# Optimization experiments

Measured on AMD Instinct MI355X. Metric: run time of the kernel, lower is better.

## Reference

```python
import jax, jax.numpy as jnp
import numpy as np
from jax import lax

B, DIM, H, W = 4, 256, 128, 128
KS, LOC, STRIDES_CFG, HEADS = 5, [2, 3], [1, 2], 8
C2 = DIM // 2
GK = HEADS * KS  # per-pixel dynamic kernel channels

def _kernel_map(ks, kstride, kloc):
    # replicates LSAMixer.generate_kernel_map_1d
    axes, strides, start = [0], [1], 1
    for loc, s in zip(kloc, kstride):
        for num in range(0, loc - start):
            axes.append(num * s + axes[-1] + strides[-1])
            strides.append(s)
        start = loc
    patch = (axes[-1] + strides[-1]) * 2 - 1
    full_axes = [-a for a in axes[:0:-1]] + axes
    full_strides = strides[:0:-1] + strides
    return full_axes, full_strides, patch

OFFS, STRDS, PATCH = _kernel_map(KS, STRIDES_CFG, LOC)
PAD = PATCH // 2

def _pw(x, w, b):
    # 1x1 conv as GEMM
    return jnp.einsum('bchw,oc->bohw', x, w) + b[None, :, None, None]

def _dw(x, w, b, ph, pw):
    # depthwise conv, torch OIHW layout with I=1
    y = lax.conv_general_dilated(x, w, (1, 1), [(ph, ph), (pw, pw)],
                                 feature_group_count=x.shape[1],
                                 dimension_numbers=('NCHW', 'OIHW', 'NCHW'))
    return y + b[None, :, None, None]

def _fsa(x, kern, groups, axis):
    # dynamic local attention: for each tap k (offset a, stride s) gather the
    # average of x over the s-wide strided window along `axis`, weight it by
    # the per-head dynamic kernel, and accumulate.
    Bx, Cx, Hx, Wx = x.shape
    gd = Cx // groups
    K = len(OFFS)
    L = x.shape[axis]
    padcfg = [(0, 0)] * 4
    padcfg[axis] = (PAD, PAD)
    xp = jnp.pad(x, padcfg)
    taps = []
    for a, s in zip(OFFS, STRDS):
        start = a if a >= 0 else a - s + 1  # window covers s pixels away from center
        acc = lax.slice_in_dim(xp, PAD + start, PAD + start + L, axis=axis)
        for d in range(1, s):
            acc = acc + lax.slice_in_dim(xp, PAD + start + d, PAD + start + d + L, axis=axis)
        taps.append(acc / s)
    t = jnp.stack(taps, 0).reshape(K, Bx, groups, gd, Hx, Wx)
    k = kern.reshape(Bx, groups, K, Hx, Wx)
    return jnp.einsum('kbgdhw,bgkhw->bgdhw', t, k).reshape(Bx, Cx, Hx, Wx)

def setup_inputs() -> dict:
    key = jax.random.key(0)
    ks = jax.random.split(key, 12)
    sc = 0.02
    f32 = jnp.float32
    return {
        'x': jax.random.normal(ks[0], (B, DIM, H, W), f32),
        'proj_in_w': jax.random.normal(ks[1], (DIM, DIM), f32) * sc,
        'proj_in_b': jnp.zeros((DIM,), f32),
        'hk_dw_w': jax.random.normal(ks[2], (C2, 1, 1, PATCH), f32) * sc,
        'hk_dw_b': jnp.zeros((C2,), f32),
        'hk_pw_w': jax.random.normal(ks[3], (GK, C2), f32) * sc,
        'hk_pw_b': jnp.zeros((GK,), f32),
        'vk_dw_w': jax.random.normal(ks[4], (C2, 1, PATCH, 1), f32) * sc,
        'vk_dw_b': jnp.zeros((C2,), f32),
        'vk_pw_w': jax.random.normal(ks[5], (GK, C2), f32) * sc,
        'vk_pw_b': jnp.zeros((GK,), f32),
        'cb_w1': jax.random.normal(ks[6], (DIM // 4, C2), f32) * sc,
        'cb_b1': jnp.zeros((DIM // 4,), f32),
        'cb_w2': jax.random.normal(ks[7], (C2, DIM // 4), f32) * sc,
        'cb_b2': jnp.zeros((C2,), f32),
        'proj_out_w': jax.random.normal(ks[8], (DIM, DIM), f32) * sc,
        'proj_out_b': jnp.zeros((DIM,), f32),
    }

def reference(x, proj_in_w, proj_in_b, hk_dw_w, hk_dw_b, hk_pw_w, hk_pw_b,
              vk_dw_w, vk_dw_b, vk_pw_w, vk_pw_b, cb_w1, cb_b1, cb_w2, cb_b2,
              proj_out_w, proj_out_b):
    Bv, _, Hv, Wv = x.shape
    h = _pw(x, proj_in_w, proj_in_b)
    x1, x2 = h[:, :C2], h[:, C2:]
    # channel branch: pw -> relu -> pw
    x_conv = _pw(jax.nn.relu(_pw(x1, cb_w1, cb_b1)), cb_w2, cb_b2)
    # horizontal dynamic kernel + fsa
    kh = jnp.tanh(_pw(_dw(x2, hk_dw_w, hk_dw_b, 0, PAD), hk_pw_w, hk_pw_b))
    attn_h = _fsa(x2, kh, HEADS, axis=3)
    # vertical dynamic kernel + fsa
    kv = jnp.tanh(_pw(_dw(attn_h, vk_dw_w, vk_dw_b, PAD, 0), vk_pw_w, vk_pw_b))
    attn = _fsa(attn_h, kv, HEADS, axis=2)
    N = Hv * Wv
    xc = x_conv.reshape(Bv, C2, N)
    at = attn.reshape(Bv, C2, N)
    # SpatialInteraction(x_conv, attn): modulates x_conv
    s_sig = jax.nn.sigmoid(jnp.einsum('bc,bcn->bn', at.mean(-1), xc) / C2)[:, None, :]
    spatial_map = (s_sig * xc).reshape(Bv, C2, Hv, Wv)
    # ChannelInteraction(x_conv, attn): modulates attn
    c_sig = jax.nn.sigmoid(jnp.einsum('bcn,bn->bc', at, xc.mean(1)) / N)[:, :, None]
    channel_map = (c_sig * at).reshape(Bv, C2, Hv, Wv)
    out = jnp.concatenate([spatial_map, channel_map], axis=1)
    return _pw(out, proj_out_w, proj_out_b)
```

## Files before the change

kernel.cpp:

```cpp
#include <hip/hip_runtime.h>
#include <hip/hip_bf16.h>
#include <math.h>

typedef __hip_bfloat16 bf16;
typedef __attribute__((ext_vector_type(8))) short short8;
typedef __attribute__((ext_vector_type(4))) float floatx4;
#define DEV __device__ __forceinline__

constexpr int BATCH = 4;
constexpr int DIM   = 256;
constexpr int C2    = 128;
constexpr int GK    = 40;
constexpr int HH    = 128;
constexpr int WW    = 128;
constexpr int NPIX  = HH * WW;
constexpr int TPB   = 256;

DEV float toF(float v) { return v; }
DEV float toF(bf16 v)  { return __bfloat162float(v); }

DEV unsigned short f2bs(float f) {
  union { bf16 h; unsigned short u; } cv;
  cv.h = __float2bfloat16(f);
  return cv.u;
}
DEV float bs2f(unsigned short u) {
  union { float f; unsigned x; } c;
  c.x = ((unsigned)u) << 16;
  return c.f;
}

template<int N>
DEV void load_f32v(const float* __restrict__ p, float* v) {
  if constexpr (N == 8) {
    const float4 a = *(const float4*)p;
    const float4 b = *(const float4*)(p + 4);
    v[0]=a.x; v[1]=a.y; v[2]=a.z; v[3]=a.w; v[4]=b.x; v[5]=b.y; v[6]=b.z; v[7]=b.w;
  } else if constexpr (N == 4) {
    const float4 a = *(const float4*)p;
    v[0]=a.x; v[1]=a.y; v[2]=a.z; v[3]=a.w;
  } else {
    const float2 a = *(const float2*)p;
    v[0]=a.x; v[1]=a.y;
  }
}
template<int N>
DEV void load_bf16v(const bf16* __restrict__ p, float* v) {
  if constexpr (N == 8) {
    const uint4 u = *(const uint4*)p;
    v[0]=bs2f(u.x & 0xffff); v[1]=bs2f(u.x >> 16);
    v[2]=bs2f(u.y & 0xffff); v[3]=bs2f(u.y >> 16);
    v[4]=bs2f(u.z & 0xffff); v[5]=bs2f(u.z >> 16);
    v[6]=bs2f(u.w & 0xffff); v[7]=bs2f(u.w >> 16);
  } else if constexpr (N == 4) {
    const uint2 u = *(const uint2*)p;
    v[0]=bs2f(u.x & 0xffff); v[1]=bs2f(u.x >> 16);
    v[2]=bs2f(u.y & 0xffff); v[3]=bs2f(u.y >> 16);
  } else {
    const unsigned u = *(const unsigned*)p;
    v[0]=bs2f(u & 0xffff); v[1]=bs2f(u >> 16);
  }
}
DEV void load8bf(const bf16* __restrict__ p, float* v) { load_bf16v<8>(p, v); }

__global__ __launch_bounds__(TPB) void prepack_kernel(
    const float* __restrict__ w0, const float* __restrict__ w1,
    const float* __restrict__ w2, const float* __restrict__ w3,
    const float* __restrict__ w4, const float* __restrict__ w5,
    short* __restrict__ dst) {
  const int i = blockIdx.x * TPB + threadIdx.x;
  if (i >= 157696) return;
  int j = i;
  float v;
  if (j < 65536) v = w0[j];
  else if ((j -= 65536) < 8192) v = w1[j];
  else if ((j -= 8192) < 8192) v = w2[j];
  else if ((j -= 8192) < 5120) v = w3[j];
  else if ((j -= 5120) < 5120) v = w4[j];
  else { j -= 5120; v = w5[j]; }
  dst[i] = (short)f2bs(v);
}

template<int K, int O, int ACT, int GATED, typename TIN, typename TOUT>
__global__ __launch_bounds__(TPB) void pw2_kernel(
    const TIN* __restrict__ in, int in_bs,
    const short* __restrict__ wbf, const float* __restrict__ bias,
    TOUT* __restrict__ out, int out_bs,
    const bf16* __restrict__ gxc, const bf16* __restrict__ gattn,
    const float* __restrict__ gs, const float* __restrict__ gc) {
  constexpr int C8   = K / 8;
  constexpr int PXT  = K / 32;
  constexpr int PG   = 64 / PXT;
  constexpr int ROWB = K * 2 + 16;
  constexpr int WO   = (O + 63) / 64;
  __shared__ char smem[64 * ROWB];

  const int p0   = blockIdx.x * 64;
  const int b    = blockIdx.y;
  const int t    = threadIdx.x;
  const int lane = t & 63, wid = t >> 6;
  const int q    = lane >> 4, i16 = lane & 15;

  {
    const int c8  = t / PG;
    const int px0 = (t % PG) * PXT;
    float vals[8][PXT];
    float svals[PXT];
    if constexpr (GATED) {
      if (c8 < C8 / 2) load_f32v<PXT>(gs + (size_t)b * NPIX + p0 + px0, svals);
    }
#pragma unroll
    for (int j = 0; j < 8; ++j) {
      const int c = c8 * 8 + j;
      float tmp[PXT];
      if constexpr (GATED) {
        if (c < C2) {
          load_bf16v<PXT>(gxc + ((size_t)b * C2 + c) * NPIX + p0 + px0, tmp);
#pragma unroll
          for (int px = 0; px < PXT; ++px) vals[j][px] = tmp[px] * svals[px];
        } else {
          const float cg = gc[b * C2 + (c - C2)];
          load_bf16v<PXT>(gattn + ((size_t)b * C2 + (c - C2)) * NPIX + p0 + px0, tmp);
#pragma unroll
          for (int px = 0; px < PXT; ++px) vals[j][px] = tmp[px] * cg;
        }
      } else {
        const TIN* src = in + ((size_t)b * in_bs + c) * NPIX + p0 + px0;
        if constexpr (sizeof(TIN) == 4) load_f32v<PXT>((const float*)src, tmp);
        else                            load_bf16v<PXT>((const bf16*)src, tmp);
#pragma unroll
        for (int px = 0; px < PXT; ++px) vals[j][px] = tmp[px];
      }
    }
#pragma unroll
    for (int px = 0; px < PXT; ++px) {
      const int p = px0 + px;
      short8 pk;
#pragma unroll
      for (int j = 0; j < 8; ++j) pk[j] = (short)f2bs(vals[j][px]);
      const int phys = c8 ^ ((p >> 3) & 7);
      *reinterpret_cast<short8*>(smem + (size_t)p * ROWB + phys * 16) = pk;
    }
  }
  __syncthreads();

  const int o_base = wid * WO * 16;
  if (o_base >= O) return;

  floatx4 acc[WO][4];
#pragma unroll
  for (int ot = 0; ot < WO; ++ot)
#pragma unroll
    for (int nt = 0; nt < 4; ++nt)
      acc[ot][nt] = (floatx4){0.f, 0.f, 0.f, 0.f};

  for (int kc = 0; kc < K / 32; ++kc) {
    short8 afrag[WO];
#pragma unroll
    for (int ot = 0; ot < WO; ++ot) {
      int o = o_base + ot * 16 + i16;
      if (o >= O) o = O - 1;
      afrag[ot] = *reinterpret_cast<const short8*>(wbf + (size_t)o * K + kc * 32 + q * 8);
    }
    short8 bfrag[4];
#pragma unroll
    for (int nt = 0; nt < 4; ++nt) {
      const int n = nt * 16 + i16;
      const int phys = (kc * 4 + q) ^ ((n >> 3) & 7);
      bfrag[nt] = *reinterpret_cast<const short8*>(smem + (size_t)n * ROWB + phys * 16);
    }
#pragma unroll
    for (int ot = 0; ot < WO; ++ot)
#pragma unroll
      for (int nt = 0; nt < 4; ++nt)
        acc[ot][nt] = __builtin_amdgcn_mfma_f32_16x16x32_bf16(
            afrag[ot], bfrag[nt], acc[ot][nt], 0, 0, 0);
  }

#pragma unroll
  for (int ot = 0; ot < WO; ++ot) {
#pragma unroll
    for (int reg = 0; reg < 4; ++reg) {
      const int o = o_base + ot * 16 + q * 4 + reg;
      if (o < O) {
        const float bv = bias[o];
#pragma unroll
        for (int nt = 0; nt < 4; ++nt) {
          float v = acc[ot][nt][reg] + bv;
          if (ACT == 1) v = fmaxf(v, 0.0f);
          if (ACT == 2) v = tanhf(v);
          TOUT* dst = out + ((size_t)b * out_bs + o) * NPIX + p0 + nt * 16 + i16;
          if constexpr (sizeof(TOUT) == 4) *dst = v;
          else *dst = __float2bfloat16(v);
        }
      }
    }
  }
}

__global__ __launch_bounds__(TPB) void dwh2_kernel(
    const float* __restrict__ in, int in_bs,
    const float* __restrict__ w7, const float* __restrict__ bias,
    bf16* __restrict__ out) {
  const int g  = blockIdx.x * TPB + threadIdx.x;
  const int w8 = g & 15;
  const int hp = (g >> 4) & (HH - 1);
  const int c  = (g >> 11) & (C2 - 1);
  const int b  = g >> 18;
  const float* xr = in + ((size_t)b * in_bs + c) * NPIX + hp * WW;
  const int px0 = w8 * 8;
  float xs[14];
  if (w8 > 0) { const float4 L = *(const float4*)(xr + px0 - 4); xs[0]=L.y; xs[1]=L.z; xs[2]=L.w; }
  else { xs[0]=xs[1]=xs[2]=0.f; }
  { const float4 a = *(const float4*)(xr + px0);
    const float4 bq = *(const float4*)(xr + px0 + 4);
    xs[3]=a.x; xs[4]=a.y; xs[5]=a.z; xs[6]=a.w;
    xs[7]=bq.x; xs[8]=bq.y; xs[9]=bq.z; xs[10]=bq.w; }
  if (w8 < 15) { const float4 R = *(const float4*)(xr + px0 + 8); xs[11]=R.x; xs[12]=R.y; xs[13]=R.z; }
  else { xs[11]=xs[12]=xs[13]=0.f; }
  float wv[7];
#pragma unroll
  for (int j = 0; j < 7; ++j) wv[j] = w7[c * 7 + j];
  const float bv = bias[c];
  short8 o;
#pragma unroll
  for (int i = 0; i < 8; ++i) {
    float a = bv;
#pragma unroll
    for (int j = 0; j < 7; ++j) a = fmaf(wv[j], xs[i + j], a);
    o[i] = (short)f2bs(a);
  }
  *reinterpret_cast<short8*>(out + ((size_t)(b * C2 + c)) * NPIX + hp * WW + px0) = o;
}

__global__ __launch_bounds__(TPB) void dwv2_kernel(
    const bf16* __restrict__ in,
    const float* __restrict__ w7, const float* __restrict__ bias,
    bf16* __restrict__ out) {
  const int g  = blockIdx.x * TPB + threadIdx.x;
  const int w8 = g & 15;
  const int hp = (g >> 4) & (HH - 1);
  const int c  = (g >> 11) & (C2 - 1);
  const int b  = g >> 18;
  const int px0 = w8 * 8;
  const bf16* base = in + ((size_t)(b * C2 + c)) * NPIX + px0;
  float r[7][8];
#pragma unroll
  for (int j = 0; j < 7; ++j) {
    const int hq = hp - 3 + j;
    if (hq >= 0 && hq < HH) load8bf(base + (size_t)hq * WW, r[j]);
    else
#pragma unroll
      for (int i = 0; i < 8; ++i) r[j][i] = 0.f;
  }
  float wv[7];
#pragma unroll
  for (int j = 0; j < 7; ++j) wv[j] = w7[c * 7 + j];
  const float bv = bias[c];
  short8 o;
#pragma unroll
  for (int i = 0; i < 8; ++i) {
    float a = bv;
#pragma unroll
    for (int j = 0; j < 7; ++j) a = fmaf(wv[j], r[j][i], a);
    o[i] = (short)f2bs(a);
  }
  *reinterpret_cast<short8*>(out + ((size_t)(b * C2 + c)) * NPIX + hp * WW + px0) = o;
}

__global__ __launch_bounds__(TPB) void fsah2_kernel(
    const float* __restrict__ x, int x_bs,
    const bf16* __restrict__ kern, bf16* __restrict__ out) {
  const int g  = blockIdx.x * TPB + threadIdx.x;
  const int w8 = g & 15;
  const int hp = (g >> 4) & (HH - 1);
  const int c  = (g >> 11) & (C2 - 1);
  const int b  = g >> 18;
  const float* xr = x + ((size_t)b * x_bs + c) * NPIX + hp * WW;
  const int px0 = w8 * 8;
  float xs[14];
  if (w8 > 0) { const float4 L = *(const float4*)(xr + px0 - 4); xs[0]=L.y; xs[1]=L.z; xs[2]=L.w; }
  else { xs[0]=xs[1]=xs[2]=0.f; }
  { const float4 a = *(const float4*)(xr + px0);
    const float4 bq = *(const float4*)(xr + px0 + 4);
    xs[3]=a.x; xs[4]=a.y; xs[5]=a.z; xs[6]=a.w;
    xs[7]=bq.x; xs[8]=bq.y; xs[9]=bq.z; xs[10]=bq.w; }
  if (w8 < 15) { const float4 R = *(const float4*)(xr + px0 + 8); xs[11]=R.x; xs[12]=R.y; xs[13]=R.z; }
  else { xs[11]=xs[12]=xs[13]=0.f; }
  float k[5][8];
  const bf16* kr = kern + ((size_t)b * GK + (c >> 4) * 5) * NPIX + hp * WW + px0;
#pragma unroll
  for (int tp = 0; tp < 5; ++tp) load8bf(kr + (size_t)tp * NPIX, k[tp]);
  short8 o;
#pragma unroll
  for (int i = 0; i < 8; ++i) {
    float a = 0.5f * (xs[i] + xs[i + 1]) * k[0][i];
    a = fmaf(xs[i + 2], k[1][i], a);
    a = fmaf(xs[i + 3], k[2][i], a);
    a = fmaf(xs[i + 4], k[3][i], a);
    a = fmaf(0.5f * (xs[i + 5] + xs[i + 6]), k[4][i], a);
    o[i] = (short)f2bs(a);
  }
  *reinterpret_cast<short8*>(out + ((size_t)(b * C2 + c)) * NPIX + hp * WW + px0) = o;
}

__global__ __launch_bounds__(TPB) void fsav2_kernel(
    const bf16* __restrict__ x,
    const bf16* __restrict__ kern, bf16* __restrict__ out) {
  const int g  = blockIdx.x * TPB + threadIdx.x;
  const int w8 = g & 15;
  const int hp = (g >> 4) & (HH - 1);
  const int c  = (g >> 11) & (C2 - 1);
  const int b  = g >> 18;
  const int px0 = w8 * 8;
  const bf16* base = x + ((size_t)(b * C2 + c)) * NPIX + px0;
  float r[7][8];
#pragma unroll
  for (int j = 0; j < 7; ++j) {
    const int hq = hp - 3 + j;
    if (hq >= 0 && hq < HH) load8bf(base + (size_t)hq * WW, r[j]);
    else
#pragma unroll
      for (int i = 0; i < 8; ++i) r[j][i] = 0.f;
  }
  float k[5][8];
  const bf16* kr = kern + ((size_t)b * GK + (c >> 4) * 5) * NPIX + hp * WW + px0;
#pragma unroll
  for (int tp = 0; tp < 5; ++tp) load8bf(kr + (size_t)tp * NPIX, k[tp]);
  short8 o;
#pragma unroll
  for (int i = 0; i < 8; ++i) {
    float a = 0.5f * (r[0][i] + r[1][i]) * k[0][i];
    a = fmaf(r[2][i], k[1][i], a);
    a = fmaf(r[3][i], k[2][i], a);
    a = fmaf(r[4][i], k[3][i], a);
    a = fmaf(0.5f * (r[5][i] + r[6][i]), k[4][i], a);
    o[i] = (short)f2bs(a);
  }
  *reinterpret_cast<short8*>(out + ((size_t)(b * C2 + c)) * NPIX + hp * WW + px0) = o;
}

DEV float block_reduce_sum(float v) {
#pragma unroll
  for (int off = 32; off > 0; off >>= 1) v += __shfl_down(v, off, 64);
  __shared__ float ls[TPB / 64];
  const int lane = threadIdx.x & 63;
  const int wid  = threadIdx.x >> 6;
  if (lane == 0) ls[wid] = v;
  __syncthreads();
  float s = 0.0f;
  if (threadIdx.x == 0) {
#pragma unroll
    for (int i = 0; i < TPB / 64; ++i) s += ls[i];
  }
  return s;
}

__global__ __launch_bounds__(TPB) void mean_n_kernel(const bf16* __restrict__ in,
                                                     float* __restrict__ out) {
  const int bc = blockIdx.x;
  const bf16* r = in + (size_t)bc * NPIX;
  float s = 0.0f;
  for (int i = threadIdx.x * 8; i < NPIX; i += TPB * 8) {
    float v[8];
    load8bf(r + i, v);
#pragma unroll
    for (int j = 0; j < 8; ++j) s += v[j];
  }
  s = block_reduce_sum(s);
  if (threadIdx.x == 0) out[bc] = s * (1.0f / NPIX);
}

__global__ __launch_bounds__(TPB) void xcmean_kernel(const bf16* __restrict__ xc,
                                                     float* __restrict__ out) {
  const int p = blockIdx.x * TPB + threadIdx.x;
  const int b = blockIdx.y;
  const bf16* r = xc + (size_t)b * C2 * NPIX + p;
  float s = 0.0f;
#pragma unroll 4
  for (int c = 0; c < C2; ++c) s += toF(r[(size_t)c * NPIX]);
  out[(size_t)b * NPIX + p] = s * (1.0f / C2);
}

__global__ __launch_bounds__(TPB) void ssig_kernel(const bf16* __restrict__ xc,
                                                   const float* __restrict__ at_mean,
                                                   float* __restrict__ out) {
  __shared__ float am[C2];
  const int b = blockIdx.y;
  if (threadIdx.x < C2) am[threadIdx.x] = at_mean[b * C2 + threadIdx.x];
  __syncthreads();
  const int p = blockIdx.x * TPB + threadIdx.x;
  const bf16* r = xc + (size_t)b * C2 * NPIX + p;
  float s = 0.0f;
#pragma unroll 4
  for (int c = 0; c < C2; ++c) s = fmaf(am[c], toF(r[(size_t)c * NPIX]), s);
  out[(size_t)b * NPIX + p] = 1.0f / (1.0f + expf(-s * (1.0f / C2)));
}

__global__ __launch_bounds__(TPB) void csig_kernel(const bf16* __restrict__ attn,
                                                   const float* __restrict__ xc_mean,
                                                   float* __restrict__ out) {
  const int bc = blockIdx.x;
  const int b  = bc / C2;
  const bf16* r = attn + (size_t)bc * NPIX;
  const float* m = xc_mean + (size_t)b * NPIX;
  float s = 0.0f;
  for (int i = threadIdx.x * 8; i < NPIX; i += TPB * 8) {
    float v[8], mm[8];
    load8bf(r + i, v);
    load_f32v<8>(m + i, mm);
#pragma unroll
    for (int j = 0; j < 8; ++j) s = fmaf(v[j], mm[j], s);
  }
  s = block_reduce_sum(s);
  if (threadIdx.x == 0) out[bc] = 1.0f / (1.0f + expf(-s * (1.0f / NPIX)));
}

extern "C" void kernel_launch(void* const* d_in, const int* in_sizes, int n_in,
                              void* d_out, int out_size, void* d_ws, size_t ws_size,
                              hipStream_t stream) {
  const float* x    = (const float*)d_in[0];
  const float* piw  = (const float*)d_in[1];
  const float* pib  = (const float*)d_in[2];
  const float* hkdw = (const float*)d_in[3];
  const float* hkdb = (const float*)d_in[4];
  const float* hkpw = (const float*)d_in[5];
  const float* hkpb = (const float*)d_in[6];
  const float* vkdw = (const float*)d_in[7];
  const float* vkdb = (const float*)d_in[8];
  const float* vkpw = (const float*)d_in[9];
  const float* vkpb = (const float*)d_in[10];
  const float* cbw1 = (const float*)d_in[11];
  const float* cbb1 = (const float*)d_in[12];
  const float* cbw2 = (const float*)d_in[13];
  const float* cbb2 = (const float*)d_in[14];
  const float* pow_ = (const float*)d_in[15];
  const float* pob  = (const float*)d_in[16];
  float* out = (float*)d_out;

  char* ws = (char*)d_ws;
  size_t off = 0;
  auto alloc = [&](size_t bytes) -> char* {
    char* p = ws + off;
    off += (bytes + 255) & ~(size_t)255;
    return p;
  };
  short* wpk    = (short*)alloc(157696 * 2);
  float* h      = (float*)alloc((size_t)BATCH * DIM * NPIX * 4);
  bf16*  t1     = (bf16*) alloc((size_t)BATCH * 64  * NPIX * 2);
  bf16*  x_conv = (bf16*) alloc((size_t)BATCH * C2  * NPIX * 2);
  bf16*  dwbuf  = (bf16*) alloc((size_t)BATCH * C2  * NPIX * 2);
  bf16*  kbuf   = (bf16*) alloc((size_t)BATCH * GK  * NPIX * 2);
  bf16*  attn_h = (bf16*) alloc((size_t)BATCH * C2  * NPIX * 2);
  bf16*  attn   = (bf16*) alloc((size_t)BATCH * C2  * NPIX * 2);
  float* at_mean = (float*)alloc((size_t)BATCH * C2 * 4);
  float* xc_mean = (float*)alloc((size_t)BATCH * NPIX * 4);
  float* s_sig   = (float*)alloc((size_t)BATCH * NPIX * 4);
  float* c_sig   = (float*)alloc((size_t)BATCH * C2 * 4);

  const short* w_pi  = wpk;
  const short* w_cb1 = wpk + 65536;
  const short* w_cb2 = wpk + 73728;
  const short* w_hk  = wpk + 81920;
  const short* w_vk  = wpk + 87040;
  const short* w_po  = wpk + 92160;

  const dim3 blk(TPB);
  const dim3 gemm_grid(NPIX / 64, BATCH);
  const int PT  = NPIX / TPB;
  const int EL8 = BATCH * C2 * HH * 16 / TPB;
  const float* x2 = h + (size_t)C2 * NPIX;

  prepack_kernel<<<dim3((157696 + TPB - 1) / TPB), blk, 0, stream>>>(
      piw, cbw1, cbw2, hkpw, vkpw, pow_, wpk);
  pw2_kernel<256, 256, 0, 0, float, float><<<gemm_grid, blk, 0, stream>>>(
      x, DIM, w_pi, pib, h, DIM, nullptr, nullptr, nullptr, nullptr);
  pw2_kernel<128, 64, 1, 0, float, bf16><<<gemm_grid, blk, 0, stream>>>(
      h, DIM, w_cb1, cbb1, t1, 64, nullptr, nullptr, nullptr, nullptr);
  pw2_kernel<64, 128, 0, 0, bf16, bf16><<<gemm_grid, blk, 0, stream>>>(
      t1, 64, w_cb2, cbb2, x_conv, C2, nullptr, nullptr, nullptr, nullptr);
  dwh2_kernel<<<dim3(EL8), blk, 0, stream>>>(x2, DIM, hkdw, hkdb, dwbuf);
  pw2_kernel<128, 40, 2, 0, bf16, bf16><<<gemm_grid, blk, 0, stream>>>(
      dwbuf, C2, w_hk, hkpb, kbuf, GK, nullptr, nullptr, nullptr, nullptr);
  fsah2_kernel<<<dim3(EL8), blk, 0, stream>>>(x2, DIM, kbuf, attn_h);
  dwv2_kernel<<<dim3(EL8), blk, 0, stream>>>(attn_h, vkdw, vkdb, dwbuf);
  pw2_kernel<128, 40, 2, 0, bf16, bf16><<<gemm_grid, blk, 0, stream>>>(
      dwbuf, C2, w_vk, vkpb, kbuf, GK, nullptr, nullptr, nullptr, nullptr);
  fsav2_kernel<<<dim3(EL8), blk, 0, stream>>>(attn_h, kbuf, attn);
  mean_n_kernel<<<dim3(BATCH * C2), blk, 0, stream>>>(attn, at_mean);
  xcmean_kernel<<<dim3(PT, BATCH), blk, 0, stream>>>(x_conv, xc_mean);
  ssig_kernel<<<dim3(PT, BATCH), blk, 0, stream>>>(x_conv, at_mean, s_sig);
  csig_kernel<<<dim3(BATCH * C2), blk, 0, stream>>>(attn, xc_mean, c_sig);
  pw2_kernel<256, 256, 0, 1, bf16, float><<<gemm_grid, blk, 0, stream>>>(
      x_conv, 0, w_po, pob, out, DIM, x_conv, attn, s_sig, c_sig);
}
```

Measured before the change: 304.9 us.

## Split output channels across blocks in big GEMMs, chunk staging, fuse xc reductions

The two 256x256 pointwise GEMMs now split their output channels across two blocks per pixel tile, which doubles the grid. Each block re-stages the same input tile into shared memory. The staging loop is processed in chunks of up to 4 pixels to cut register pressure, and launch bounds now request 4 blocks per CU to raise occupancy. The xc mean and spatial sigmoid kernels are fused into one pass over x_conv, which removes a full read of that tensor. The cost is duplicated input loads and conversion work in the split GEMMs.

Result: slower. 316.1 us (+3.7%).

```diff
diff --git a/kernel.cpp b/kernel.cpp
--- a/kernel.cpp
+++ b/kernel.cpp
@@ -81,8 +81,8 @@
   dst[i] = (short)f2bs(v);
 }
 
-template<int K, int O, int ACT, int GATED, typename TIN, typename TOUT>
-__global__ __launch_bounds__(TPB) void pw2_kernel(
+template<int K, int O, int OSPL, int ACT, int GATED, typename TIN, typename TOUT>
+__global__ __launch_bounds__(TPB, 4) void pw2_kernel(
     const TIN* __restrict__ in, int in_bs,
     const short* __restrict__ wbf, const float* __restrict__ bias,
     TOUT* __restrict__ out, int out_bs,
@@ -92,10 +92,14 @@
   constexpr int PXT  = K / 32;
   constexpr int PG   = 64 / PXT;
   constexpr int ROWB = K * 2 + 16;
-  constexpr int WO   = (O + 63) / 64;
+  constexpr int OB   = O / OSPL;
+  constexpr int WO   = (OB + 63) / 64;
+  constexpr int CH   = (PXT < 4) ? PXT : 4;
   __shared__ char smem[64 * ROWB];
 
-  const int p0   = blockIdx.x * 64;
+  const int bx   = blockIdx.x;
+  const int oz   = (OSPL > 1) ? (bx % OSPL) : 0;
+  const int p0   = ((OSPL > 1) ? (bx / OSPL) : bx) * 64;
   const int b    = blockIdx.y;
   const int t    = threadIdx.x;
   const int lane = t & 63, wid = t >> 6;
@@ -104,48 +108,51 @@
   {
     const int c8  = t / PG;
     const int px0 = (t % PG) * PXT;
-    float vals[8][PXT];
-    float svals[PXT];
-    if constexpr (GATED) {
-      if (c8 < C8 / 2) load_f32v<PXT>(gs + (size_t)b * NPIX + p0 + px0, svals);
-    }
-#pragma unroll
-    for (int j = 0; j < 8; ++j) {
-      const int c = c8 * 8 + j;
-      float tmp[PXT];
+#pragma unroll
+    for (int pc = 0; pc < PXT; pc += CH) {
+      float vals[8][CH];
+      float svals[CH];
       if constexpr (GATED) {
-        if (c < C2) {
-          load_bf16v<PXT>(gxc + ((size_t)b * C2 + c) * NPIX + p0 + px0, tmp);
-#pragma unroll
-          for (int px = 0; px < PXT; ++px) vals[j][px] = tmp[px] * svals[px];
+        if (c8 < C8 / 2) load_f32v<CH>(gs + (size_t)b * NPIX + p0 + px0 + pc, svals);
+      }
+#pragma unroll
+      for (int j = 0; j < 8; ++j) {
+        const int c = c8 * 8 + j;
+        float tmp[CH];
+        if constexpr (GATED) {
+          if (c < C2) {
+            load_bf16v<CH>(gxc + ((size_t)b * C2 + c) * NPIX + p0 + px0 + pc, tmp);
+#pragma unroll
+            for (int px = 0; px < CH; ++px) vals[j][px] = tmp[px] * svals[px];
+          } else {
+            const float cg = gc[b * C2 + (c - C2)];
+            load_bf16v<CH>(gattn + ((size_t)b * C2 + (c - C2)) * NPIX + p0 + px0 + pc, tmp);
+#pragma unroll
+            for (int px = 0; px < CH; ++px) vals[j][px] = tmp[px] * cg;
+          }
         } else {
-          const float cg = gc[b * C2 + (c - C2)];
-          load_bf16v<PXT>(gattn + ((size_t)b * C2 + (c - C2)) * NPIX + p0 + px0, tmp);
-#pragma unroll
-          for (int px = 0; px < PXT; ++px) vals[j][px] = tmp[px] * cg;
+          const TIN* src = in + ((size_t)b * in_bs + c) * NPIX + p0 + px0 + pc;
+          if constexpr (sizeof(TIN) == 4) load_f32v<CH>((const float*)src, tmp);
+          else                            load_bf16v<CH>((const bf16*)src, tmp);
+#pragma unroll
+          for (int px = 0; px < CH; ++px) vals[j][px] = tmp[px];
         }
-      } else {
-        const TIN* src = in + ((size_t)b * in_bs + c) * NPIX + p0 + px0;
-        if constexpr (sizeof(TIN) == 4) load_f32v<PXT>((const float*)src, tmp);
-        else                            load_bf16v<PXT>((const bf16*)src, tmp);
-#pragma unroll
-        for (int px = 0; px < PXT; ++px) vals[j][px] = tmp[px];
+      }
+#pragma unroll
+      for (int px = 0; px < CH; ++px) {
+        const int p = px0 + pc + px;
+        short8 pk;
+#pragma unroll
+        for (int j = 0; j < 8; ++j) pk[j] = (short)f2bs(vals[j][px]);
+        const int phys = c8 ^ ((p >> 3) & 7);
+        *reinterpret_cast<short8*>(smem + (size_t)p * ROWB + phys * 16) = pk;
       }
     }
-#pragma unroll
-    for (int px = 0; px < PXT; ++px) {
-      const int p = px0 + px;
-      short8 pk;
-#pragma unroll
-      for (int j = 0; j < 8; ++j) pk[j] = (short)f2bs(vals[j][px]);
-      const int phys = c8 ^ ((p >> 3) & 7);
-      *reinterpret_cast<short8*>(smem + (size_t)p * ROWB + phys * 16) = pk;
-    }
   }
   __syncthreads();
 
-  const int o_base = wid * WO * 16;
-  if (o_base >= O) return;
+  if (wid * WO * 16 >= OB) return;
+  const int o_base = oz * OB + wid * WO * 16;
 
   floatx4 acc[WO][4];
 #pragma unroll
@@ -371,30 +378,25 @@
   if (threadIdx.x == 0) out[bc] = s * (1.0f / NPIX);
 }
 
-__global__ __launch_bounds__(TPB) void xcmean_kernel(const bf16* __restrict__ xc,
-                                                     float* __restrict__ out) {
-  const int p = blockIdx.x * TPB + threadIdx.x;
-  const int b = blockIdx.y;
-  const bf16* r = xc + (size_t)b * C2 * NPIX + p;
-  float s = 0.0f;
-#pragma unroll 4
-  for (int c = 0; c < C2; ++c) s += toF(r[(size_t)c * NPIX]);
-  out[(size_t)b * NPIX + p] = s * (1.0f / C2);
-}
-
-__global__ __launch_bounds__(TPB) void ssig_kernel(const bf16* __restrict__ xc,
-                                                   const float* __restrict__ at_mean,
-                                                   float* __restrict__ out) {
+__global__ __launch_bounds__(TPB) void xs_kernel(const bf16* __restrict__ xc,
+                                                 const float* __restrict__ at_mean,
+                                                 float* __restrict__ xc_mean,
+                                                 float* __restrict__ s_sig) {
   __shared__ float am[C2];
   const int b = blockIdx.y;
   if (threadIdx.x < C2) am[threadIdx.x] = at_mean[b * C2 + threadIdx.x];
   __syncthreads();
   const int p = blockIdx.x * TPB + threadIdx.x;
   const bf16* r = xc + (size_t)b * C2 * NPIX + p;
-  float s = 0.0f;
+  float s = 0.0f, m = 0.0f;
 #pragma unroll 4
-  for (int c = 0; c < C2; ++c) s = fmaf(am[c], toF(r[(size_t)c * NPIX]), s);
-  out[(size_t)b * NPIX + p] = 1.0f / (1.0f + expf(-s * (1.0f / C2)));
+  for (int c = 0; c < C2; ++c) {
+    const float v = toF(r[(size_t)c * NPIX]);
+    m += v;
+    s = fmaf(am[c], v, s);
+  }
+  xc_mean[(size_t)b * NPIX + p] = m * (1.0f / C2);
+  s_sig[(size_t)b * NPIX + p]   = 1.0f / (1.0f + expf(-s * (1.0f / C2)));
 }
 
 __global__ __launch_bounds__(TPB) void csig_kernel(const bf16* __restrict__ attn,
@@ -467,30 +469,30 @@
 
   const dim3 blk(TPB);
   const dim3 gemm_grid(NPIX / 64, BATCH);
+  const dim3 gemm_grid2(NPIX / 64 * 2, BATCH);
   const int PT  = NPIX / TPB;
   const int EL8 = BATCH * C2 * HH * 16 / TPB;
   const float* x2 = h + (size_t)C2 * NPIX;
 
   prepack_kernel<<<dim3((157696 + TPB - 1) / TPB), blk, 0, stream>>>(
       piw, cbw1, cbw2, hkpw, vkpw, pow_, wpk);
-  pw2_kernel<256, 256, 0, 0, float, float><<<gemm_grid, blk, 0, stream>>>(
+  pw2_kernel<256, 256, 2, 0, 0, float, float><<<gemm_grid2, blk, 0, stream>>>(
       x, DIM, w_pi, pib, h, DIM, nullptr, nullptr, nullptr, nullptr);
-  pw2_kernel<128, 64, 1, 0, float, bf16><<<gemm_grid, blk, 0, stream>>>(
+  pw2_kernel<128, 64, 1, 1, 0, float, bf16><<<gemm_grid, blk, 0, stream>>>(
       h, DIM, w_cb1, cbb1, t1, 64, nullptr, nullptr, nullptr, nullptr);
-  pw2_kernel<64, 128, 0, 0, bf16, bf16><<<gemm_grid, blk, 0, stream>>>(
+  pw2_kernel<64, 128, 1, 0, 0, bf16, bf16><<<gemm_grid, blk, 0, stream>>>(
       t1, 64, w_cb2, cbb2, x_conv, C2, nullptr, nullptr, nullptr, nullptr);
   dwh2_kernel<<<dim3(EL8), blk, 0, stream>>>(x2, DIM, hkdw, hkdb, dwbuf);
-  pw2_kernel<128, 40, 2, 0, bf16, bf16><<<gemm_grid, blk, 0, stream>>>(
+  pw2_kernel<128, 40, 1, 2, 0, bf16, bf16><<<gemm_grid, blk, 0, stream>>>(
       dwbuf, C2, w_hk, hkpb, kbuf, GK, nullptr, nullptr, nullptr, nullptr);
   fsah2_kernel<<<dim3(EL8), blk, 0, stream>>>(x2, DIM, kbuf, attn_h);
   dwv2_kernel<<<dim3(EL8), blk, 0, stream>>>(attn_h, vkdw, vkdb, dwbuf);
-  pw2_kernel<128, 40, 2, 0, bf16, bf16><<<gemm_grid, blk, 0, stream>>>(
+  pw2_kernel<128, 40, 1, 2, 0, bf16, bf16><<<gemm_grid, blk, 0, stream>>>(
       dwbuf, C2, w_vk, vkpb, kbuf, GK, nullptr, nullptr, nullptr, nullptr);
   fsav2_kernel<<<dim3(EL8), blk, 0, stream>>>(attn_h, kbuf, attn);
   mean_n_kernel<<<dim3(BATCH * C2), blk, 0, stream>>>(attn, at_mean);
-  xcmean_kernel<<<dim3(PT, BATCH), blk, 0, stream>>>(x_conv, xc_mean);
-  ssig_kernel<<<dim3(PT, BATCH), blk, 0, stream>>>(x_conv, at_mean, s_sig);
+  xs_kernel<<<dim3(PT, BATCH), blk, 0, stream>>>(x_conv, at_mean, xc_mean, s_sig);
   csig_kernel<<<dim3(BATCH * C2), blk, 0, stream>>>(attn, xc_mean, c_sig);
-  pw2_kernel<256, 256, 0, 1, bf16, float><<<gemm_grid, blk, 0, stream>>>(
+  pw2_kernel<256, 256, 2, 0, 1, bf16, float><<<gemm_grid2, blk, 0, stream>>>(
       x_conv, 0, w_po, pob, out, DIM, x_conv, attn, s_sig, c_sig);
 }
```

## Double-buffer pointwise GEMM tiles and fuse xc-mean with spatial sigmoid

Applied to the files above, without the earlier changes.

Each pointwise-conv GEMM block now processes two 64-pixel tiles and ping-pongs between two shared-memory buffers. The global loads for the next tile are issued before the MFMA compute on the current tile, so load latency can overlap with math. The launch grid is halved to match. Separately, the xc_mean and s_sig reductions over x_conv are merged into one kernel, so x_conv is read once and one launch is dropped. The trade-offs are more register pressure from keeping prefetched values live, with launch_bounds now asking for 2 blocks per CU, doubled LDS per block, and fewer blocks in flight.

New measurement: 314.8 us. +3.3%, slower.

```diff
diff --git a/kernel.cpp b/kernel.cpp
--- a/kernel.cpp
+++ b/kernel.cpp
@@ -81,8 +81,8 @@
   dst[i] = (short)f2bs(v);
 }
 
-template<int K, int O, int ACT, int GATED, typename TIN, typename TOUT>
-__global__ __launch_bounds__(TPB) void pw2_kernel(
+template<int K, int O, int T, int ACT, int GATED, typename TIN, typename TOUT>
+__global__ __launch_bounds__(TPB, 2) void pw3_kernel(
     const TIN* __restrict__ in, int in_bs,
     const short* __restrict__ wbf, const float* __restrict__ bias,
     TOUT* __restrict__ out, int out_bs,
@@ -92,19 +92,21 @@
   constexpr int PXT  = K / 32;
   constexpr int PG   = 64 / PXT;
   constexpr int ROWB = K * 2 + 16;
+  constexpr int BUFB = 64 * ROWB;
   constexpr int WO   = (O + 63) / 64;
-  __shared__ char smem[64 * ROWB];
-
-  const int p0   = blockIdx.x * 64;
+  __shared__ char smem[2 * BUFB];
+
   const int b    = blockIdx.y;
   const int t    = threadIdx.x;
   const int lane = t & 63, wid = t >> 6;
   const int q    = lane >> 4, i16 = lane & 15;
-
-  {
-    const int c8  = t / PG;
-    const int px0 = (t % PG) * PXT;
-    float vals[8][PXT];
+  const int c8   = t / PG;
+  const int px0  = (t % PG) * PXT;
+  const int o_base = wid * WO * 16;
+
+  float vals[8][PXT];
+
+  auto stage_load = [&](int p0) {
     float svals[PXT];
     if constexpr (GATED) {
       if (c8 < C8 / 2) load_f32v<PXT>(gs + (size_t)b * NPIX + p0 + px0, svals);
@@ -112,8 +114,8 @@
 #pragma unroll
     for (int j = 0; j < 8; ++j) {
       const int c = c8 * 8 + j;
-      float tmp[PXT];
       if constexpr (GATED) {
+        float tmp[PXT];
         if (c < C2) {
           load_bf16v<PXT>(gxc + ((size_t)b * C2 + c) * NPIX + p0 + px0, tmp);
 #pragma unroll
@@ -126,12 +128,13 @@
         }
       } else {
         const TIN* src = in + ((size_t)b * in_bs + c) * NPIX + p0 + px0;
-        if constexpr (sizeof(TIN) == 4) load_f32v<PXT>((const float*)src, tmp);
-        else                            load_bf16v<PXT>((const bf16*)src, tmp);
-#pragma unroll
-        for (int px = 0; px < PXT; ++px) vals[j][px] = tmp[px];
+        if constexpr (sizeof(TIN) == 4) load_f32v<PXT>((const float*)src, vals[j]);
+        else                            load_bf16v<PXT>((const bf16*)src, vals[j]);
       }
     }
+  };
+
+  auto stage_write = [&](char* buf) {
 #pragma unroll
     for (int px = 0; px < PXT; ++px) {
       const int p = px0 + px;
@@ -139,62 +142,73 @@
 #pragma unroll
       for (int j = 0; j < 8; ++j) pk[j] = (short)f2bs(vals[j][px]);
       const int phys = c8 ^ ((p >> 3) & 7);
-      *reinterpret_cast<short8*>(smem + (size_t)p * ROWB + phys * 16) = pk;
+      *reinterpret_cast<short8*>(buf + (size_t)p * ROWB + phys * 16) = pk;
     }
-  }
-  __syncthreads();
-
-  const int o_base = wid * WO * 16;
-  if (o_base >= O) return;
-
-  floatx4 acc[WO][4];
-#pragma unroll
-  for (int ot = 0; ot < WO; ++ot)
-#pragma unroll
-    for (int nt = 0; nt < 4; ++nt)
-      acc[ot][nt] = (floatx4){0.f, 0.f, 0.f, 0.f};
-
-  for (int kc = 0; kc < K / 32; ++kc) {
-    short8 afrag[WO];
+  };
+
+  auto compute_store = [&](const char* buf, int p0) {
+    floatx4 acc[WO][4];
+#pragma unroll
+    for (int ot = 0; ot < WO; ++ot)
+#pragma unroll
+      for (int nt = 0; nt < 4; ++nt)
+        acc[ot][nt] = (floatx4){0.f, 0.f, 0.f, 0.f};
+
+    for (int kc = 0; kc < K / 32; ++kc) {
+      short8 afrag[WO];
+#pragma unroll
+      for (int ot = 0; ot < WO; ++ot) {
+        int o = o_base + ot * 16 + i16;
+        if (o >= O) o = O - 1;
+        afrag[ot] = *reinterpret_cast<const short8*>(wbf + (size_t)o * K + kc * 32 + q * 8);
+      }
+      short8 bfrag[4];
+#pragma unroll
+      for (int nt = 0; nt < 4; ++nt) {
+        const int n = nt * 16 + i16;
+        const int phys = (kc * 4 + q) ^ ((n >> 3) & 7);
+        bfrag[nt] = *reinterpret_cast<const short8*>(buf + (size_t)n * ROWB + phys * 16);
+      }
+#pragma unroll
+      for (int ot = 0; ot < WO; ++ot)
+#pragma unroll
+        for (int nt = 0; nt < 4; ++nt)
+          acc[ot][nt] = __builtin_amdgcn_mfma_f32_16x16x32_bf16(
+              afrag[ot], bfrag[nt], acc[ot][nt], 0, 0, 0);
+    }
+
 #pragma unroll
     for (int ot = 0; ot < WO; ++ot) {
-      int o = o_base + ot * 16 + i16;
-      if (o >= O) o = O - 1;
-      afrag[ot] = *reinterpret_cast<const short8*>(wbf + (size_t)o * K + kc * 32 + q * 8);
-    }
-    short8 bfrag[4];
-#pragma unroll
-    for (int nt = 0; nt < 4; ++nt) {
-      const int n = nt * 16 + i16;
-      const int phys = (kc * 4 + q) ^ ((n >> 3) & 7);
-      bfrag[nt] = *reinterpret_cast<const short8*>(smem + (size_t)n * ROWB + phys * 16);
-    }
-#pragma unroll
-    for (int ot = 0; ot < WO; ++ot)
-#pragma unroll
-      for (int nt = 0; nt < 4; ++nt)
-        acc[ot][nt] = __builtin_amdgcn_mfma_f32_16x16x32_bf16(
-            afrag[ot], bfrag[nt], acc[ot][nt], 0, 0, 0);
-  }
-
-#pragma unroll
-  for (int ot = 0; ot < WO; ++ot) {
-#pragma unroll
-    for (int reg = 0; reg < 4; ++reg) {
-      const int o = o_base + ot * 16 + q * 4 + reg;
-      if (o < O) {
-        const float bv = bias[o];
-#pragma unroll
-        for (int nt = 0; nt < 4; ++nt) {
-          float v = acc[ot][nt][reg] + bv;
-          if (ACT == 1) v = fmaxf(v, 0.0f);
-          if (ACT == 2) v = tanhf(v);
-          TOUT* dst = out + ((size_t)b * out_bs + o) * NPIX + p0 + nt * 16 + i16;
-          if constexpr (sizeof(TOUT) == 4) *dst = v;
-          else *dst = __float2bfloat16(v);
+#pragma unroll
+      for (int reg = 0; reg < 4; ++reg) {
+        const int o = o_base + ot * 16 + q * 4 + reg;
+        if (o < O) {
+          const float bv = bias[o];
+#pragma unroll
+          for (int nt = 0; nt < 4; ++nt) {
+            float v = acc[ot][nt][reg] + bv;
+            if (ACT == 1) v = fmaxf(v, 0.0f);
+            if (ACT == 2) v = tanhf(v);
+            TOUT* dst = out + ((size_t)b * out_bs + o) * NPIX + p0 + nt * 16 + i16;
+            if constexpr (sizeof(TOUT) == 4) *dst = v;
+            else *dst = __float2bfloat16(v);
+          }
         }
       }
     }
+  };
+
+  const int p_base = blockIdx.x * T * 64;
+
+  stage_load(p_base);
+  stage_write(smem);
+  __syncthreads();
+
+  for (int tt = 0; tt < T; ++tt) {
+    if (tt + 1 < T) stage_load(p_base + (tt + 1) * 64);
+    if (o_base < O) compute_store(smem + (tt & 1) * BUFB, p_base + tt * 64);
+    if (tt + 1 < T) stage_write(smem + ((tt + 1) & 1) * BUFB);
+    __syncthreads();
   }
 }
 
@@ -371,30 +385,25 @@
   if (threadIdx.x == 0) out[bc] = s * (1.0f / NPIX);
 }
 
-__global__ __launch_bounds__(TPB) void xcmean_kernel(const bf16* __restrict__ xc,
-                                                     float* __restrict__ out) {
-  const int p = blockIdx.x * TPB + threadIdx.x;
-  const int b = blockIdx.y;
-  const bf16* r = xc + (size_t)b * C2 * NPIX + p;
-  float s = 0.0f;
-#pragma unroll 4
-  for (int c = 0; c < C2; ++c) s += toF(r[(size_t)c * NPIX]);
-  out[(size_t)b * NPIX + p] = s * (1.0f / C2);
-}
-
-__global__ __launch_bounds__(TPB) void ssig_kernel(const bf16* __restrict__ xc,
-                                                   const float* __restrict__ at_mean,
-                                                   float* __restrict__ out) {
+__global__ __launch_bounds__(TPB) void xs_kernel(const bf16* __restrict__ xc,
+                                                 const float* __restrict__ at_mean,
+                                                 float* __restrict__ xc_mean,
+                                                 float* __restrict__ s_sig) {
   __shared__ float am[C2];
   const int b = blockIdx.y;
   if (threadIdx.x < C2) am[threadIdx.x] = at_mean[b * C2 + threadIdx.x];
   __syncthreads();
   const int p = blockIdx.x * TPB + threadIdx.x;
   const bf16* r = xc + (size_t)b * C2 * NPIX + p;
-  float s = 0.0f;
+  float s = 0.0f, m = 0.0f;
 #pragma unroll 4
-  for (int c = 0; c < C2; ++c) s = fmaf(am[c], toF(r[(size_t)c * NPIX]), s);
-  out[(size_t)b * NPIX + p] = 1.0f / (1.0f + expf(-s * (1.0f / C2)));
+  for (int c = 0; c < C2; ++c) {
+    const float v = toF(r[(size_t)c * NPIX]);
+    m += v;
+    s = fmaf(am[c], v, s);
+  }
+  xc_mean[(size_t)b * NPIX + p] = m * (1.0f / C2);
+  s_sig[(size_t)b * NPIX + p]   = 1.0f / (1.0f + expf(-s * (1.0f / C2)));
 }
 
 __global__ __launch_bounds__(TPB) void csig_kernel(const bf16* __restrict__ attn,
@@ -466,31 +475,31 @@
   const short* w_po  = wpk + 92160;
 
   const dim3 blk(TPB);
-  const dim3 gemm_grid(NPIX / 64, BATCH);
+  constexpr int TLS = 2;
+  const dim3 gemm_grid(NPIX / 64 / TLS, BATCH);
   const int PT  = NPIX / TPB;
   const int EL8 = BATCH * C2 * HH * 16 / TPB;
   const float* x2 = h + (size_t)C2 * NPIX;
 
   prepack_kernel<<<dim3((157696 + TPB - 1) / TPB), blk, 0, stream>>>(
       piw, cbw1, cbw2, hkpw, vkpw, pow_, wpk);
-  pw2_kernel<256, 256, 0, 0, float, float><<<gemm_grid, blk, 0, stream>>>(
+  pw3_kernel<256, 256, TLS, 0, 0, float, float><<<gemm_grid, blk, 0, stream>>>(
       x, DIM, w_pi, pib, h, DIM, nullptr, nullptr, nullptr, nullptr);
-  pw2_kernel<128, 64, 1, 0, float, bf16><<<gemm_grid, blk, 0, stream>>>(
+  pw3_kernel<128, 64, TLS, 1, 0, float, bf16><<<gemm_grid, blk, 0, stream>>>(
       h, DIM, w_cb1, cbb1, t1, 64, nullptr, nullptr, nullptr, nullptr);
-  pw2_kernel<64, 128, 0, 0, bf16, bf16><<<gemm_grid, blk, 0, stream>>>(
+  pw3_kernel<64, 128, TLS, 0, 0, bf16, bf16><<<gemm_grid, blk, 0, stream>>>(
       t1, 64, w_cb2, cbb2, x_conv, C2, nullptr, nullptr, nullptr, nullptr);
   dwh2_kernel<<<dim3(EL8), blk, 0, stream>>>(x2, DIM, hkdw, hkdb, dwbuf);
-  pw2_kernel<128, 40, 2, 0, bf16, bf16><<<gemm_grid, blk, 0, stream>>>(
+  pw3_kernel<128, 40, TLS, 2, 0, bf16, bf16><<<gemm_grid, blk, 0, stream>>>(
       dwbuf, C2, w_hk, hkpb, kbuf, GK, nullptr, nullptr, nullptr, nullptr);
   fsah2_kernel<<<dim3(EL8), blk, 0, stream>>>(x2, DIM, kbuf, attn_h);
   dwv2_kernel<<<dim3(EL8), blk, 0, stream>>>(attn_h, vkdw, vkdb, dwbuf);
-  pw2_kernel<128, 40, 2, 0, bf16, bf16><<<gemm_grid, blk, 0, stream>>>(
+  pw3_kernel<128, 40, TLS, 2, 0, bf16, bf16><<<gemm_grid, blk, 0, stream>>>(
       dwbuf, C2, w_vk, vkpb, kbuf, GK, nullptr, nullptr, nullptr, nullptr);
   fsav2_kernel<<<dim3(EL8), blk, 0, stream>>>(attn_h, kbuf, attn);
   mean_n_kernel<<<dim3(BATCH * C2), blk, 0, stream>>>(attn, at_mean);
-  xcmean_kernel<<<dim3(PT, BATCH), blk, 0, stream>>>(x_conv, xc_mean);
-  ssig_kernel<<<dim3(PT, BATCH), blk, 0, stream>>>(x_conv, at_mean, s_sig);
+  xs_kernel<<<dim3(PT, BATCH), blk, 0, stream>>>(x_conv, at_mean, xc_mean, s_sig);
   csig_kernel<<<dim3(BATCH * C2), blk, 0, stream>>>(attn, xc_mean, c_sig);
-  pw2_kernel<256, 256, 0, 1, bf16, float><<<gemm_grid, blk, 0, stream>>>(
+  pw3_kernel<256, 256, TLS, 0, 1, bf16, float><<<gemm_grid, blk, 0, stream>>>(
       x_conv, 0, w_po, pob, out, DIM, x_conv, attn, s_sig, c_sig);
 }
```

## Fuse proj_in and channel-branch GEMMs into one kernel; merge xc mean and spatial sigmoid

Applied to the files above, without the earlier changes.

Adds a single kernel that runs the input projection, the first channel-branch pointwise conv with ReLU, and the second pointwise conv back to back. The x1 half and the intermediate t1 stay in shared memory as bf16, so the full fp32 h tensor and t1 are never written to or re-read from global memory. Only x2 is written out in fp32 for the later depthwise and attention stages. It also merges the xc mean and s_sig reductions into one pass over x_conv. The cost is a larger shared-memory footprint per block, which may lower occupancy.

Measured after the change: 283.9 us. 1.07x faster.

```diff
diff --git a/kernel.cpp b/kernel.cpp
--- a/kernel.cpp
+++ b/kernel.cpp
@@ -193,6 +193,191 @@
           if constexpr (sizeof(TOUT) == 4) *dst = v;
           else *dst = __float2bfloat16(v);
         }
+      }
+    }
+  }
+}
+
+__global__ __launch_bounds__(TPB) void pwfused_kernel(
+    const float* __restrict__ x,
+    const short* __restrict__ w_pi, const float* __restrict__ pib,
+    const short* __restrict__ w_cb1, const float* __restrict__ cbb1,
+    const short* __restrict__ w_cb2, const float* __restrict__ cbb2,
+    float* __restrict__ x2out, bf16* __restrict__ xconv) {
+  constexpr int ROWB  = 256 * 2 + 16;
+  constexpr int HROWB = 128 * 2 + 16;
+  constexpr int TROWB = 64 * 2 + 16;
+  __shared__ char smem[64 * ROWB];
+  __shared__ char hbuf[64 * HROWB];
+  __shared__ char tbuf[64 * TROWB];
+
+  const int p0   = blockIdx.x * 64;
+  const int b    = blockIdx.y;
+  const int t    = threadIdx.x;
+  const int lane = t & 63, wid = t >> 6;
+  const int q    = lane >> 4, i16 = lane & 15;
+
+  {
+    const int c8  = t / 8;
+    const int px0 = (t % 8) * 8;
+    float vals[8][8];
+#pragma unroll
+    for (int j = 0; j < 8; ++j) {
+      const int c = c8 * 8 + j;
+      load_f32v<8>(x + ((size_t)b * DIM + c) * NPIX + p0 + px0, vals[j]);
+    }
+#pragma unroll
+    for (int px = 0; px < 8; ++px) {
+      const int p = px0 + px;
+      short8 pk;
+#pragma unroll
+      for (int j = 0; j < 8; ++j) pk[j] = (short)f2bs(vals[j][px]);
+      const int phys = c8 ^ ((p >> 3) & 7);
+      *reinterpret_cast<short8*>(smem + (size_t)p * ROWB + phys * 16) = pk;
+    }
+  }
+  __syncthreads();
+
+  const int o_base = wid * 64;
+  {
+    floatx4 acc[4][4];
+#pragma unroll
+    for (int ot = 0; ot < 4; ++ot)
+#pragma unroll
+      for (int nt = 0; nt < 4; ++nt)
+        acc[ot][nt] = (floatx4){0.f, 0.f, 0.f, 0.f};
+
+    for (int kc = 0; kc < 8; ++kc) {
+      short8 afrag[4];
+#pragma unroll
+      for (int ot = 0; ot < 4; ++ot) {
+        const int o = o_base + ot * 16 + i16;
+        afrag[ot] = *reinterpret_cast<const short8*>(w_pi + (size_t)o * 256 + kc * 32 + q * 8);
+      }
+      short8 bfrag[4];
+#pragma unroll
+      for (int nt = 0; nt < 4; ++nt) {
+        const int n = nt * 16 + i16;
+        const int phys = (kc * 4 + q) ^ ((n >> 3) & 7);
+        bfrag[nt] = *reinterpret_cast<const short8*>(smem + (size_t)n * ROWB + phys * 16);
+      }
+#pragma unroll
+      for (int ot = 0; ot < 4; ++ot)
+#pragma unroll
+        for (int nt = 0; nt < 4; ++nt)
+          acc[ot][nt] = __builtin_amdgcn_mfma_f32_16x16x32_bf16(
+              afrag[ot], bfrag[nt], acc[ot][nt], 0, 0, 0);
+    }
+
+#pragma unroll
+    for (int ot = 0; ot < 4; ++ot) {
+      const int ch0 = o_base + ot * 16 + q * 4;
+      if (ch0 >= C2) {
+#pragma unroll
+        for (int reg = 0; reg < 4; ++reg) {
+          const int o = ch0 + reg;
+          const float bv = pib[o];
+#pragma unroll
+          for (int nt = 0; nt < 4; ++nt)
+            x2out[((size_t)b * C2 + (o - C2)) * NPIX + p0 + nt * 16 + i16] =
+                acc[ot][nt][reg] + bv;
+        }
+      } else {
+        float bv4[4];
+#pragma unroll
+        for (int reg = 0; reg < 4; ++reg) bv4[reg] = pib[ch0 + reg];
+#pragma unroll
+        for (int nt = 0; nt < 4; ++nt) {
+          const int px = nt * 16 + i16;
+          ushort4 pk;
+          pk.x = f2bs(acc[ot][nt][0] + bv4[0]);
+          pk.y = f2bs(acc[ot][nt][1] + bv4[1]);
+          pk.z = f2bs(acc[ot][nt][2] + bv4[2]);
+          pk.w = f2bs(acc[ot][nt][3] + bv4[3]);
+          const int phys = (ch0 >> 3) ^ ((px >> 3) & 7);
+          *reinterpret_cast<ushort4*>(hbuf + (size_t)px * HROWB + phys * 16 +
+                                      (ch0 & 7) * 2) = pk;
+        }
+      }
+    }
+  }
+  __syncthreads();
+
+  {
+    floatx4 acc2[4];
+#pragma unroll
+    for (int nt = 0; nt < 4; ++nt) acc2[nt] = (floatx4){0.f, 0.f, 0.f, 0.f};
+    const int o2b = wid * 16;
+    for (int kc = 0; kc < 4; ++kc) {
+      const short8 afrag = *reinterpret_cast<const short8*>(
+          w_cb1 + (size_t)(o2b + i16) * 128 + kc * 32 + q * 8);
+      short8 bfrag[4];
+#pragma unroll
+      for (int nt = 0; nt < 4; ++nt) {
+        const int n = nt * 16 + i16;
+        const int phys = (kc * 4 + q) ^ ((n >> 3) & 7);
+        bfrag[nt] = *reinterpret_cast<const short8*>(hbuf + (size_t)n * HROWB + phys * 16);
+      }
+#pragma unroll
+      for (int nt = 0; nt < 4; ++nt)
+        acc2[nt] = __builtin_amdgcn_mfma_f32_16x16x32_bf16(afrag, bfrag[nt], acc2[nt], 0, 0, 0);
+    }
+    const int ch0 = o2b + q * 4;
+    float bv4[4];
+#pragma unroll
+    for (int reg = 0; reg < 4; ++reg) bv4[reg] = cbb1[ch0 + reg];
+#pragma unroll
+    for (int nt = 0; nt < 4; ++nt) {
+      const int px = nt * 16 + i16;
+      ushort4 pk;
+      pk.x = f2bs(fmaxf(acc2[nt][0] + bv4[0], 0.f));
+      pk.y = f2bs(fmaxf(acc2[nt][1] + bv4[1], 0.f));
+      pk.z = f2bs(fmaxf(acc2[nt][2] + bv4[2], 0.f));
+      pk.w = f2bs(fmaxf(acc2[nt][3] + bv4[3], 0.f));
+      const int phys = (ch0 >> 3) ^ ((px >> 3) & 7);
+      *reinterpret_cast<ushort4*>(tbuf + (size_t)px * TROWB + phys * 16 +
+                                  (ch0 & 7) * 2) = pk;
+    }
+  }
+  __syncthreads();
+
+  {
+    floatx4 acc3[2][4];
+#pragma unroll
+    for (int ot = 0; ot < 2; ++ot)
+#pragma unroll
+      for (int nt = 0; nt < 4; ++nt) acc3[ot][nt] = (floatx4){0.f, 0.f, 0.f, 0.f};
+    const int o3b = wid * 32;
+    for (int kc = 0; kc < 2; ++kc) {
+      short8 afrag[2];
+#pragma unroll
+      for (int ot = 0; ot < 2; ++ot)
+        afrag[ot] = *reinterpret_cast<const short8*>(
+            w_cb2 + (size_t)(o3b + ot * 16 + i16) * 64 + kc * 32 + q * 8);
+      short8 bfrag[4];
+#pragma unroll
+      for (int nt = 0; nt < 4; ++nt) {
+        const int n = nt * 16 + i16;
+        const int phys = (kc * 4 + q) ^ ((n >> 3) & 7);
+        bfrag[nt] = *reinterpret_cast<const short8*>(tbuf + (size_t)n * TROWB + phys * 16);
+      }
+#pragma unroll
+      for (int ot = 0; ot < 2; ++ot)
+#pragma unroll
+        for (int nt = 0; nt < 4; ++nt)
+          acc3[ot][nt] = __builtin_amdgcn_mfma_f32_16x16x32_bf16(
+              afrag[ot], bfrag[nt], acc3[ot][nt], 0, 0, 0);
+    }
+#pragma unroll
+    for (int ot = 0; ot < 2; ++ot) {
+#pragma unroll
+      for (int reg = 0; reg < 4; ++reg) {
+        const int o = o3b + ot * 16 + q * 4 + reg;
+        const float bv = cbb2[o];
+#pragma unroll
+        for (int nt = 0; nt < 4; ++nt)
+          xconv[((size_t)b * C2 + o) * NPIX + p0 + nt * 16 + i16] =
+              __float2bfloat16(acc3[ot][nt][reg] + bv);
       }
     }
   }
@@ -371,30 +556,25 @@
   if (threadIdx.x == 0) out[bc] = s * (1.0f / NPIX);
 }
 
-__global__ __launch_bounds__(TPB) void xcmean_kernel(const bf16* __restrict__ xc,
-                                                     float* __restrict__ out) {
-  const int p = blockIdx.x * TPB + threadIdx.x;
-  const int b = blockIdx.y;
-  const bf16* r = xc + (size_t)b * C2 * NPIX + p;
-  float s = 0.0f;
-#pragma unroll 4
-  for (int c = 0; c < C2; ++c) s += toF(r[(size_t)c * NPIX]);
-  out[(size_t)b * NPIX + p] = s * (1.0f / C2);
-}
-
-__global__ __launch_bounds__(TPB) void ssig_kernel(const bf16* __restrict__ xc,
-                                                   const float* __restrict__ at_mean,
-                                                   float* __restrict__ out) {
+__global__ __launch_bounds__(TPB) void xs_kernel(const bf16* __restrict__ xc,
+                                                 const float* __restrict__ at_mean,
+                                                 float* __restrict__ xc_mean,
+                                                 float* __restrict__ s_sig) {
   __shared__ float am[C2];
   const int b = blockIdx.y;
   if (threadIdx.x < C2) am[threadIdx.x] = at_mean[b * C2 + threadIdx.x];
   __syncthreads();
   const int p = blockIdx.x * TPB + threadIdx.x;
   const bf16* r = xc + (size_t)b * C2 * NPIX + p;
-  float s = 0.0f;
+  float s = 0.0f, m = 0.0f;
 #pragma unroll 4
-  for (int c = 0; c < C2; ++c) s = fmaf(am[c], toF(r[(size_t)c * NPIX]), s);
-  out[(size_t)b * NPIX + p] = 1.0f / (1.0f + expf(-s * (1.0f / C2)));
+  for (int c = 0; c < C2; ++c) {
+    const float v = toF(r[(size_t)c * NPIX]);
+    m += v;
+    s = fmaf(am[c], v, s);
+  }
+  xc_mean[(size_t)b * NPIX + p] = m * (1.0f / C2);
+  s_sig[(size_t)b * NPIX + p]   = 1.0f / (1.0f + expf(-s * (1.0f / C2)));
 }
 
 __global__ __launch_bounds__(TPB) void csig_kernel(const bf16* __restrict__ attn,
@@ -446,8 +626,7 @@
     return p;
   };
   short* wpk    = (short*)alloc(157696 * 2);
-  float* h      = (float*)alloc((size_t)BATCH * DIM * NPIX * 4);
-  bf16*  t1     = (bf16*) alloc((size_t)BATCH * 64  * NPIX * 2);
+  float* x2buf  = (float*)alloc((size_t)BATCH * C2  * NPIX * 4);
   bf16*  x_conv = (bf16*) alloc((size_t)BATCH * C2  * NPIX * 2);
   bf16*  dwbuf  = (bf16*) alloc((size_t)BATCH * C2  * NPIX * 2);
   bf16*  kbuf   = (bf16*) alloc((size_t)BATCH * GK  * NPIX * 2);
@@ -469,27 +648,21 @@
   const dim3 gemm_grid(NPIX / 64, BATCH);
   const int PT  = NPIX / TPB;
   const int EL8 = BATCH * C2 * HH * 16 / TPB;
-  const float* x2 = h + (size_t)C2 * NPIX;
 
   prepack_kernel<<<dim3((157696 + TPB - 1) / TPB), blk, 0, stream>>>(
       piw, cbw1, cbw2, hkpw, vkpw, pow_, wpk);
-  pw2_kernel<256, 256, 0, 0, float, float><<<gemm_grid, blk, 0, stream>>>(
-      x, DIM, w_pi, pib, h, DIM, nullptr, nullptr, nullptr, nullptr);
-  pw2_kernel<128, 64, 1, 0, float, bf16><<<gemm_grid, blk, 0, stream>>>(
-      h, DIM, w_cb1, cbb1, t1, 64, nullptr, nullptr, nullptr, nullptr);
-  pw2_kernel<64, 128, 0, 0, bf16, bf16><<<gemm_grid, blk, 0, stream>>>(
-      t1, 64, w_cb2, cbb2, x_conv, C2, nullptr, nullptr, nullptr, nullptr);
-  dwh2_kernel<<<dim3(EL8), blk, 0, stream>>>(x2, DIM, hkdw, hkdb, dwbuf);
+  pwfused_kernel<<<gemm_grid, blk, 0, stream>>>(
+      x, w_pi, pib, w_cb1, cbb1, w_cb2, cbb2, x2buf, x_conv);
+  dwh2_kernel<<<dim3(EL8), blk, 0, stream>>>(x2buf, C2, hkdw, hkdb, dwbuf);
   pw2_kernel<128, 40, 2, 0, bf16, bf16><<<gemm_grid, blk, 0, stream>>>(
       dwbuf, C2, w_hk, hkpb, kbuf, GK, nullptr, nullptr, nullptr, nullptr);
-  fsah2_kernel<<<dim3(EL8), blk, 0, stream>>>(x2, DIM, kbuf, attn_h);
+  fsah2_kernel<<<dim3(EL8), blk, 0, stream>>>(x2buf, C2, kbuf, attn_h);
   dwv2_kernel<<<dim3(EL8), blk, 0, stream>>>(attn_h, vkdw, vkdb, dwbuf);
   pw2_kernel<128, 40, 2, 0, bf16, bf16><<<gemm_grid, blk, 0, stream>>>(
       dwbuf, C2, w_vk, vkpb, kbuf, GK, nullptr, nullptr, nullptr, nullptr);
   fsav2_kernel<<<dim3(EL8), blk, 0, stream>>>(attn_h, kbuf, attn);
   mean_n_kernel<<<dim3(BATCH * C2), blk, 0, stream>>>(attn, at_mean);
-  xcmean_kernel<<<dim3(PT, BATCH), blk, 0, stream>>>(x_conv, xc_mean);
-  ssig_kernel<<<dim3(PT, BATCH), blk, 0, stream>>>(x_conv, at_mean, s_sig);
+  xs_kernel<<<dim3(PT, BATCH), blk, 0, stream>>>(x_conv, at_mean, xc_mean, s_sig);
   csig_kernel<<<dim3(BATCH * C2), blk, 0, stream>>>(attn, xc_mean, c_sig);
   pw2_kernel<256, 256, 0, 1, bf16, float><<<gemm_grid, blk, 0, stream>>>(
       x_conv, 0, w_po, pob, out, DIM, x_conv, attn, s_sig, c_sig);
```
